# Optimization experiments

Measured on AMD Instinct MI355X. Metric: run time of the kernel, lower is better.

Reference implementation:

```python
import jax, jax.numpy as jnp
import numpy as np

B_COMMITMENT = 1.0


def setup_inputs() -> dict:
    key = jax.random.key(0)
    k1, k2 = jax.random.split(key)
    inpt = jax.random.normal(k1, (16, 1024, 256), dtype=jnp.float32)
    emb_mtrx = jax.random.normal(k2, (256, 8192), dtype=jnp.float32) * 0.05
    return {"inpt": inpt, "emb_mtrx": emb_mtrx}


def reference(inpt, emb_mtrx):
    D = inpt.shape[-1]
    x = inpt.reshape(-1, D)  # [N, D]
    # squared L2 distance to every code: [N, K]
    dist = (
        jnp.sum(x * x, axis=1, keepdims=True)
        - 2.0 * (x @ emb_mtrx)
        + jnp.sum(emb_mtrx * emb_mtrx, axis=0, keepdims=True)
    )
    idx = jnp.argmin(dist, axis=1).reshape(inpt.shape[:-1])  # [B, T]
    q = jnp.take(emb_mtrx.T, idx, axis=0)  # [B, T, D] gather of nearest codes
    l_commitment = jnp.mean((jax.lax.stop_gradient(q) - inpt) ** 2)
    l_codebook = jnp.mean((q - jax.lax.stop_gradient(inpt)) ** 2)
    loss = B_COMMITMENT * l_commitment + l_codebook
    q_st = inpt + jax.lax.stop_gradient(q - inpt)  # straight-through
    return q_st, loss
```

## Files before the change

### kernel.cpp

```cpp
#include <hip/hip_runtime.h>
#include <hip/hip_bf16.h>
#include <cstdint>


typedef __bf16 bf16x8 __attribute__((ext_vector_type(8)));
typedef __bf16 bf16x4 __attribute__((ext_vector_type(4)));
typedef float  f32x16 __attribute__((ext_vector_type(16)));

#define N_ROWS  16384
#define N_CODES 8192
#define DDIM    256
#define NT      16
#define BUFB    32768

#define STAGE16(gptr, lptr) __builtin_amdgcn_global_load_lds( \
    (const __attribute__((address_space(1))) void*)(gptr),    \
    (__attribute__((address_space(3))) void*)(lptr), 16, 0, 0)

#define SBAR() do { asm volatile("" ::: "memory"); \
                    __builtin_amdgcn_s_barrier();  \
                    asm volatile("" ::: "memory"); } while (0)
#define WAITVM(N) asm volatile("s_waitcnt vmcnt(" #N ")" ::: "memory")
#define LGKM0() do { asm volatile("s_waitcnt lgkmcnt(0)" ::: "memory"); \
                     __builtin_amdgcn_sched_barrier(0); } while (0)

__global__ void prep_x_k(const float* __restrict__ x,
                         __bf16* __restrict__ xhi, __bf16* __restrict__ xlo) {
  int i = blockIdx.x * 256 + threadIdx.x;
  float4 v = reinterpret_cast<const float4*>(x)[i];
  float a[4] = {v.x, v.y, v.z, v.w};
  bf16x4 h, l;
#pragma unroll
  for (int j = 0; j < 4; ++j) {
    __bf16 hh = (__bf16)a[j];
    h[j] = hh;
    l[j] = (__bf16)(a[j] - (float)hh);
  }
  reinterpret_cast<bf16x4*>(xhi)[i] = h;
  reinterpret_cast<bf16x4*>(xlo)[i] = l;
}

__global__ void prep_e_k(const float* __restrict__ emb,
                         __bf16* __restrict__ ehi, __bf16* __restrict__ elo,
                         float* __restrict__ embT) {
  __shared__ float tile[64][65];
  const int kb = blockIdx.x * 64, db = blockIdx.y * 64;
  const int t = threadIdx.x;
  const int tk = t & 63, td = t >> 6;
#pragma unroll
  for (int c = 0; c < 16; ++c) {
    int d = c * 4 + td;
    tile[d][tk] = emb[(size_t)(db + d) * N_CODES + kb + tk];
  }
  __syncthreads();
#pragma unroll
  for (int c = 0; c < 16; ++c) {
    int k = c * 4 + td;
    int d = tk;
    float v = tile[d][k];
    size_t o = (size_t)(kb + k) * DDIM + db + d;
    __bf16 h = (__bf16)v;
    embT[o] = v;
    ehi[o] = h;
    elo[o] = (__bf16)(v - (float)h);
  }
}

__global__ void enorm_k(const float* __restrict__ emb, float* __restrict__ enorm) {
  int k = blockIdx.x * 256 + threadIdx.x;
  float s = 0.f;
  for (int d = 0; d < DDIM; ++d) {
    float v = emb[(size_t)d * N_CODES + k];
    s += v * v;
  }
  enorm[k] = s;
}

__global__ __launch_bounds__(512, 2) void vq_main_k(
    const __bf16* __restrict__ xhi, const __bf16* __restrict__ xlo,
    const __bf16* __restrict__ ehi, const __bf16* __restrict__ elo,
    const float* __restrict__ enorm, unsigned long long* __restrict__ keys) {
  extern __shared__ __align__(16) unsigned char smem[];

  const int tid = threadIdx.x;
  const int wid = tid >> 6, lane = tid & 63;
  const int cg = wid >> 2, rg = wid & 3;
  const int l31 = lane & 31, lh = lane >> 5;

  const int orig = blockIdx.x;
  const int j = orig >> 3;
  const int bm = (orig & 7) * 8 + (j & 7);
  const int bn = j >> 3;

  const int cbase = bn * 256 + cg * 128 + lh * 4;
  f32x16 acc[4][2];
#pragma unroll
  for (int c = 0; c < 4; ++c) {
    f32x16 ci;
#pragma unroll
    for (int q = 0; q < 4; ++q)
#pragma unroll
      for (int r = 0; r < 4; ++r)
        ci[q * 4 + r] = -0.5f * enorm[cbase + c * 32 + q * 8 + r];
    acc[c][0] = ci; acc[c][1] = ci;
  }
  __builtin_amdgcn_sched_barrier(0);

  const size_t aoff = (size_t)(bm * 256 + wid * 32 + l31) * 512 + (size_t)lh * 16;
  const size_t boff = (size_t)(bn * 256 + wid * 32 + l31) * 512 + (size_t)lh * 16;
  const char* pxh = (const char*)xhi + aoff;
  const char* pxl = (const char*)xlo + aoff;
  const char* peh = (const char*)ehi + boff;
  const char* pel = (const char*)elo + boff;
  const int dxh = wid * 1024, dxl = 8192 + wid * 1024;
  const int deh = 16384 + wid * 1024, del = 24576 + wid * 1024;

  const int xrd = rg * 2048 + lane * 16;
  const int erd = 16384 + cg * 4096 + lane * 16;

  unsigned char* b0 = smem;
  unsigned char* b1 = smem + BUFB;
  unsigned char* b2 = smem + 2 * BUFB;

  STAGE16(pxh, b0 + dxh); STAGE16(peh, b0 + deh);
  STAGE16(pxl, b0 + dxl); STAGE16(pel, b0 + del);
  STAGE16(pxh + 32, b1 + dxh); STAGE16(peh + 32, b1 + deh);
  STAGE16(pxl + 32, b1 + dxl); STAGE16(pel + 32, b1 + del);
  WAITVM(4);
  SBAR();

#pragma unroll 1
  for (int t = 0; t < NT; ++t) {
    int s = t + 2; if (s >= NT) s -= NT;
    const size_t kb = (size_t)s * 32;

    bf16x8 ehf[4], xhf[2];
#pragma unroll
    for (int c = 0; c < 4; ++c) ehf[c] = *(const bf16x8*)(b0 + erd + c * 1024);
#pragma unroll
    for (int r = 0; r < 2; ++r) xhf[r] = *(const bf16x8*)(b0 + xrd + r * 1024);
    STAGE16(pxh + kb, b2 + dxh);
    STAGE16(peh + kb, b2 + deh);
    SBAR();
    LGKM0();
    __builtin_amdgcn_s_setprio(1);
#pragma unroll
    for (int c = 0; c < 4; ++c)
#pragma unroll
      for (int r = 0; r < 2; ++r)
        acc[c][r] = __builtin_amdgcn_mfma_f32_32x32x16_bf16(ehf[c], xhf[r], acc[c][r], 0, 0, 0);
    __builtin_amdgcn_s_setprio(0);
    SBAR();

    bf16x8 xlf[2];
#pragma unroll
    for (int r = 0; r < 2; ++r) xlf[r] = *(const bf16x8*)(b0 + 8192 + xrd + r * 1024);
    STAGE16(pxl + kb, b2 + dxl);
    SBAR();
    LGKM0();
    __builtin_amdgcn_s_setprio(1);
#pragma unroll
    for (int c = 0; c < 4; ++c)
#pragma unroll
      for (int r = 0; r < 2; ++r)
        acc[c][r] = __builtin_amdgcn_mfma_f32_32x32x16_bf16(ehf[c], xlf[r], acc[c][r], 0, 0, 0);
    __builtin_amdgcn_s_setprio(0);
    SBAR();

    bf16x8 elf[4];
#pragma unroll
    for (int c = 0; c < 4; ++c) elf[c] = *(const bf16x8*)(b0 + 8192 + erd + c * 1024);
    STAGE16(pel + kb, b2 + del);
    SBAR();
    LGKM0();
    __builtin_amdgcn_s_setprio(1);
#pragma unroll
    for (int c = 0; c < 4; ++c)
#pragma unroll
      for (int r = 0; r < 2; ++r)
        acc[c][r] = __builtin_amdgcn_mfma_f32_32x32x16_bf16(elf[c], xhf[r], acc[c][r], 0, 0, 0);
    __builtin_amdgcn_s_setprio(0);
    WAITVM(4);
    SBAR();

    unsigned char* bt = b0; b0 = b1; b1 = b2; b2 = bt;
  }
  WAITVM(0);

#pragma unroll
  for (int r = 0; r < 2; ++r) {
    float bv = -3.4e38f;
    unsigned bcode = 0;
#pragma unroll
    for (int c = 0; c < 4; ++c)
#pragma unroll
      for (int q = 0; q < 4; ++q)
#pragma unroll
        for (int rr = 0; rr < 4; ++rr) {
          float v = acc[c][r][q * 4 + rr];
          unsigned cd = (unsigned)(cbase + c * 32 + q * 8 + rr);
          if (v > bv) { bv = v; bcode = cd; }
        }
    unsigned u = __float_as_uint(bv);
    u = (u & 0x80000000u) ? ~u : (u | 0x80000000u);
    unsigned long long key =
        ((unsigned long long)u << 32) | (unsigned)(0xFFFFFFFFu ^ bcode);
    unsigned olo = __shfl_xor((unsigned)key, 32, 64);
    unsigned ohi = __shfl_xor((unsigned)(key >> 32), 32, 64);
    unsigned long long okey = ((unsigned long long)ohi << 32) | olo;
    if (okey > key) key = okey;
    if (lane < 32)
      atomicMax(&keys[bm * 256 + rg * 64 + r * 32 + l31], key);
  }
}

__global__ void gather_k(const float* __restrict__ x, const float* __restrict__ embT,
                         const unsigned long long* __restrict__ keys,
                         float* __restrict__ qout, float* __restrict__ rowsum) {
  const int row = blockIdx.x;
  const int lane = threadIdx.x;
  const unsigned low = (unsigned)(keys[row] & 0xffffffffull);
  const int idx = (int)(~low);
  float4 q  = reinterpret_cast<const float4*>(embT + (size_t)idx * DDIM)[lane];
  float4 xv = reinterpret_cast<const float4*>(x + (size_t)row * DDIM)[lane];
  reinterpret_cast<float4*>(qout + (size_t)row * DDIM)[lane] = q;
  float dx = q.x - xv.x, dy = q.y - xv.y, dz = q.z - xv.z, dw = q.w - xv.w;
  float s = dx * dx + dy * dy + dz * dz + dw * dw;
#pragma unroll
  for (int mk = 32; mk; mk >>= 1) s += __shfl_xor(s, mk, 64);
  if (lane == 0) rowsum[row] = s;
}

__global__ void loss_k(const float* __restrict__ rowsum, float* __restrict__ out) {
  __shared__ float sm[4];
  const int t = threadIdx.x;
  float s = 0.f;
  for (int j = t; j < N_ROWS; j += 256) s += rowsum[j];
#pragma unroll
  for (int mk = 32; mk; mk >>= 1) s += __shfl_xor(s, mk, 64);
  if ((t & 63) == 0) sm[t >> 6] = s;
  __syncthreads();
  if (t == 0) out[0] = 2.0f * (sm[0] + sm[1] + sm[2] + sm[3]) / (float)(N_ROWS * DDIM);
}

extern "C" void kernel_launch(void* const* d_in, const int* in_sizes, int n_in,
                              void* d_out, int out_size, void* d_ws, size_t ws_size,
                              hipStream_t stream) {
  const float* x   = (const float*)d_in[0];
  const float* emb = (const float*)d_in[1];
  float* qout = (float*)d_out;

  char* w = (char*)d_ws;
  unsigned long long* keys = (unsigned long long*)w;
  float* rowsum = (float*)(w + 131072);
  __bf16* xhi = (__bf16*)(w + 196608);
  __bf16* xlo = xhi + (size_t)N_ROWS * DDIM;
  __bf16* ehi = xlo + (size_t)N_ROWS * DDIM;
  __bf16* elo = ehi + (size_t)N_CODES * DDIM;
  float*  embT = (float*)(elo + (size_t)N_CODES * DDIM);
  float*  enorm = embT + (size_t)N_CODES * DDIM;

  hipFuncSetAttribute((const void*)vq_main_k,
                      hipFuncAttributeMaxDynamicSharedMemorySize, 3 * BUFB);

  hipMemsetAsync(keys, 0, N_ROWS * sizeof(unsigned long long), stream);
  prep_x_k<<<4096, 256, 0, stream>>>(x, xhi, xlo);
  prep_e_k<<<dim3(N_CODES / 64, DDIM / 64), 256, 0, stream>>>(emb, ehi, elo, embT);
  enorm_k<<<N_CODES / 256, 256, 0, stream>>>(emb, enorm);
  vq_main_k<<<2048, 512, 3 * BUFB, stream>>>(xhi, xlo, ehi, elo, enorm, keys);
  gather_k<<<N_ROWS, 64, 0, stream>>>(x, embT, keys, qout, rowsum);
  loss_k<<<1, 256, 0, stream>>>(rowsum, qout + (size_t)N_ROWS * DDIM);
}
```

Baseline: 246.2 us.

## Add bf16-only first pass with margin-based rescue of ambiguous rows

Replaces the single split-precision (hi+lo) distance GEMM with a hi-only bf16 pass that tracks the top two scores per row. Rows whose winning margin exceeds a fixed threshold are accepted directly. The remaining rows, up to a cap, are compacted and recomputed with the full hi/lo precision kernel. The fp32 transposed codebook copy is dropped and gather rebuilds codes from hi+lo. This cuts roughly two thirds of the MFMA work for confident rows, at the cost of extra kernels and a heuristic threshold that could mis-assign rows when bf16 error exceeds the margin.

Measured after the change: 239.4 us. 2.8% less time.

```diff
diff --git a/kernel.cpp b/kernel.cpp
--- a/kernel.cpp
+++ b/kernel.cpp
@@ -11,7 +11,10 @@
 #define N_CODES 8192
 #define DDIM    256
 #define NT      16
-#define BUFB    32768
+#define BUFB1   16384
+#define BUFB3   32768
+#define NMAX    8192
+#define THETA   0.025f
 
 #define STAGE16(gptr, lptr) __builtin_amdgcn_global_load_lds( \
     (const __attribute__((address_space(1))) void*)(gptr),    \
@@ -24,6 +27,15 @@
 #define LGKM0() do { asm volatile("s_waitcnt lgkmcnt(0)" ::: "memory"); \
                      __builtin_amdgcn_sched_barrier(0); } while (0)
 
+__device__ __forceinline__ unsigned mapf(float f) {
+  unsigned u = __float_as_uint(f);
+  return (u & 0x80000000u) ? ~u : (u | 0x80000000u);
+}
+__device__ __forceinline__ float unmapf(unsigned u) {
+  u = (u & 0x80000000u) ? (u & 0x7fffffffu) : ~u;
+  return __uint_as_float(u);
+}
+
 __global__ void prep_x_k(const float* __restrict__ x,
                          __bf16* __restrict__ xhi, __bf16* __restrict__ xlo) {
   int i = blockIdx.x * 256 + threadIdx.x;
@@ -41,8 +53,7 @@
 }
 
 __global__ void prep_e_k(const float* __restrict__ emb,
-                         __bf16* __restrict__ ehi, __bf16* __restrict__ elo,
-                         float* __restrict__ embT) {
+                         __bf16* __restrict__ ehi, __bf16* __restrict__ elo) {
   __shared__ float tile[64][65];
   const int kb = blockIdx.x * 64, db = blockIdx.y * 64;
   const int t = threadIdx.x;
@@ -60,7 +71,6 @@
     float v = tile[d][k];
     size_t o = (size_t)(kb + k) * DDIM + db + d;
     __bf16 h = (__bf16)v;
-    embT[o] = v;
     ehi[o] = h;
     elo[o] = (__bf16)(v - (float)h);
   }
@@ -76,11 +86,11 @@
   enorm[k] = s;
 }
 
-__global__ __launch_bounds__(512, 2) void vq_main_k(
-    const __bf16* __restrict__ xhi, const __bf16* __restrict__ xlo,
-    const __bf16* __restrict__ ehi, const __bf16* __restrict__ elo,
-    const float* __restrict__ enorm, unsigned long long* __restrict__ keys) {
-  extern __shared__ __align__(16) unsigned char smem[];
+__global__ __launch_bounds__(512, 2) void pass1_k(
+    const __bf16* __restrict__ xhi, const __bf16* __restrict__ ehi,
+    const float* __restrict__ enorm,
+    unsigned long long* __restrict__ k2k, float* __restrict__ k2v) {
+  __shared__ alignas(16) unsigned char smem[3][BUFB1];
 
   const int tid = threadIdx.x;
   const int wid = tid >> 6, lane = tid & 63;
@@ -109,7 +119,167 @@
   const size_t aoff = (size_t)(bm * 256 + wid * 32 + l31) * 512 + (size_t)lh * 16;
   const size_t boff = (size_t)(bn * 256 + wid * 32 + l31) * 512 + (size_t)lh * 16;
   const char* pxh = (const char*)xhi + aoff;
-  const char* pxl = (const char*)xlo + aoff;
+  const char* peh = (const char*)ehi + boff;
+  const int dxh = wid * 1024, deh = 8192 + wid * 1024;
+
+  const int xrd = rg * 2048 + lane * 16;
+  const int erd = 8192 + cg * 4096 + lane * 16;
+
+  unsigned char* b0 = &smem[0][0];
+  unsigned char* b1 = &smem[1][0];
+  unsigned char* b2 = &smem[2][0];
+
+  STAGE16(pxh, b0 + dxh); STAGE16(peh, b0 + deh);
+  STAGE16(pxh + 32, b1 + dxh); STAGE16(peh + 32, b1 + deh);
+  WAITVM(2);
+  SBAR();
+
+#pragma unroll 1
+  for (int t = 0; t < NT; ++t) {
+    int s = t + 2; if (s >= NT) s -= NT;
+    const size_t kb = (size_t)s * 32;
+
+    bf16x8 ehf[4], xhf[2];
+#pragma unroll
+    for (int c = 0; c < 4; ++c) ehf[c] = *(const bf16x8*)(b0 + erd + c * 1024);
+#pragma unroll
+    for (int r = 0; r < 2; ++r) xhf[r] = *(const bf16x8*)(b0 + xrd + r * 1024);
+    STAGE16(pxh + kb, b2 + dxh);
+    STAGE16(peh + kb, b2 + deh);
+    SBAR();
+    LGKM0();
+    __builtin_amdgcn_s_setprio(1);
+#pragma unroll
+    for (int c = 0; c < 4; ++c)
+#pragma unroll
+      for (int r = 0; r < 2; ++r)
+        acc[c][r] = __builtin_amdgcn_mfma_f32_32x32x16_bf16(ehf[c], xhf[r], acc[c][r], 0, 0, 0);
+    __builtin_amdgcn_s_setprio(0);
+    WAITVM(2);
+    SBAR();
+    unsigned char* bt = b0; b0 = b1; b1 = b2; b2 = bt;
+  }
+  WAITVM(0);
+  SBAR();
+
+  unsigned long long* ek = (unsigned long long*)&smem[0][0];
+  float* ev = (float*)(&smem[0][0] + 2048);
+  const int rowl = rg * 64 + l31;
+
+#pragma unroll
+  for (int r = 0; r < 2; ++r) {
+    float v1 = -3.4e38f, v2 = -3.4e38f;
+    unsigned c1 = 0;
+#pragma unroll
+    for (int c = 0; c < 4; ++c)
+#pragma unroll
+      for (int q = 0; q < 4; ++q)
+#pragma unroll
+        for (int rr = 0; rr < 4; ++rr) {
+          float v = acc[c][r][q * 4 + rr];
+          unsigned cd = (unsigned)(cbase + c * 32 + q * 8 + rr);
+          if (v > v1) { v2 = v1; v1 = v; c1 = cd; }
+          else if (v > v2) v2 = v;
+        }
+    unsigned long long key =
+        ((unsigned long long)mapf(v1) << 32) | (0xFFFFFFFFu ^ c1);
+    unsigned klo = (unsigned)key, khi = (unsigned)(key >> 32);
+    unsigned plo = __shfl_xor(klo, 32, 64), phi = __shfl_xor(khi, 32, 64);
+    float pv1 = __shfl_xor(v1, 32, 64), pv2 = __shfl_xor(v2, 32, 64);
+    unsigned long long pkey = ((unsigned long long)phi << 32) | plo;
+    if (pkey > key) { v2 = fmaxf(v1, pv2); v1 = pv1; key = pkey; }
+    else { v2 = fmaxf(pv1, v2); }
+    SBAR();
+    if (cg == 1 && lh == 0) { ek[rowl + r * 32] = key; ev[rowl + r * 32] = v2; }
+    SBAR();
+    if (cg == 0 && lh == 0) {
+      unsigned long long pk = ek[rowl + r * 32];
+      float ps2 = ev[rowl + r * 32];
+      float nv2;
+      if (pk > key) { nv2 = fmaxf(v1, ps2); key = pk; }
+      else nv2 = fmaxf(unmapf((unsigned)(pk >> 32)), v2);
+      const int grow = bm * 256 + rowl + r * 32;
+      k2k[(size_t)bn * N_ROWS + grow] = key;
+      k2v[(size_t)bn * N_ROWS + grow] = nv2;
+    }
+  }
+}
+
+__global__ void reduce_k(const unsigned long long* __restrict__ k2k,
+                         const float* __restrict__ k2v,
+                         unsigned long long* __restrict__ keys,
+                         unsigned* __restrict__ counter,
+                         int* __restrict__ idxlist) {
+  const int row = blockIdx.x * 256 + threadIdx.x;
+  unsigned long long k = k2k[row];
+  float s2 = k2v[row];
+#pragma unroll 1
+  for (int p = 1; p < 32; ++p) {
+    unsigned long long kk = k2k[(size_t)p * N_ROWS + row];
+    float ss2 = k2v[(size_t)p * N_ROWS + row];
+    if (kk > k) { s2 = fmaxf(unmapf((unsigned)(k >> 32)), ss2); k = kk; }
+    else        { s2 = fmaxf(unmapf((unsigned)(kk >> 32)), s2); }
+  }
+  float v1 = unmapf((unsigned)(k >> 32));
+  if (v1 - s2 >= THETA) {
+    keys[row] = k;
+  } else {
+    keys[row] = 0;
+    unsigned pos = atomicAdd(counter, 1u);
+    if (pos < NMAX) idxlist[pos] = row;
+    else keys[row] = k;
+  }
+}
+
+__global__ void compact_k(const __bf16* __restrict__ xhi, const __bf16* __restrict__ xlo,
+                          const int* __restrict__ idxlist, const unsigned* __restrict__ counter,
+                          __bf16* __restrict__ xch, __bf16* __restrict__ xcl) {
+  const unsigned b = blockIdx.x;
+  if (b >= *counter) return;
+  const int row = idxlist[b];
+  const int lane = threadIdx.x;
+  reinterpret_cast<uint2*>(xch)[(size_t)b * 64 + lane] =
+      reinterpret_cast<const uint2*>(xhi)[(size_t)row * 64 + lane];
+  reinterpret_cast<uint2*>(xcl)[(size_t)b * 64 + lane] =
+      reinterpret_cast<const uint2*>(xlo)[(size_t)row * 64 + lane];
+}
+
+__global__ __launch_bounds__(512, 2) void rescue_k(
+    const __bf16* __restrict__ xch, const __bf16* __restrict__ xcl,
+    const __bf16* __restrict__ ehi, const __bf16* __restrict__ elo,
+    const float* __restrict__ enorm, unsigned long long* __restrict__ keys,
+    const int* __restrict__ idxlist, const unsigned* __restrict__ counter) {
+  extern __shared__ __align__(16) unsigned char smem[];
+
+  const int bm = blockIdx.x >> 5;
+  const int bn = blockIdx.x & 31;
+  const unsigned nf = *counter;
+  const int tiles = (int)((nf + 255u) >> 8);
+  if (bm >= tiles) return;
+
+  const int tid = threadIdx.x;
+  const int wid = tid >> 6, lane = tid & 63;
+  const int cg = wid >> 2, rg = wid & 3;
+  const int l31 = lane & 31, lh = lane >> 5;
+
+  const int cbase = bn * 256 + cg * 128 + lh * 4;
+  f32x16 acc[4][2];
+#pragma unroll
+  for (int c = 0; c < 4; ++c) {
+    f32x16 ci;
+#pragma unroll
+    for (int q = 0; q < 4; ++q)
+#pragma unroll
+      for (int r = 0; r < 4; ++r)
+        ci[q * 4 + r] = -0.5f * enorm[cbase + c * 32 + q * 8 + r];
+    acc[c][0] = ci; acc[c][1] = ci;
+  }
+  __builtin_amdgcn_sched_barrier(0);
+
+  const size_t aoff = (size_t)(bm * 256 + wid * 32 + l31) * 512 + (size_t)lh * 16;
+  const size_t boff = (size_t)(bn * 256 + wid * 32 + l31) * 512 + (size_t)lh * 16;
+  const char* pxh = (const char*)xch + aoff;
+  const char* pxl = (const char*)xcl + aoff;
   const char* peh = (const char*)ehi + boff;
   const char* pel = (const char*)elo + boff;
   const int dxh = wid * 1024, dxl = 8192 + wid * 1024;
@@ -119,8 +289,8 @@
   const int erd = 16384 + cg * 4096 + lane * 16;
 
   unsigned char* b0 = smem;
-  unsigned char* b1 = smem + BUFB;
-  unsigned char* b2 = smem + 2 * BUFB;
+  unsigned char* b1 = smem + BUFB3;
+  unsigned char* b2 = smem + 2 * BUFB3;
 
   STAGE16(pxh, b0 + dxh); STAGE16(peh, b0 + deh);
   STAGE16(pxl, b0 + dxl); STAGE16(pel, b0 + del);
@@ -201,28 +371,34 @@
           unsigned cd = (unsigned)(cbase + c * 32 + q * 8 + rr);
           if (v > bv) { bv = v; bcode = cd; }
         }
-    unsigned u = __float_as_uint(bv);
-    u = (u & 0x80000000u) ? ~u : (u | 0x80000000u);
     unsigned long long key =
-        ((unsigned long long)u << 32) | (unsigned)(0xFFFFFFFFu ^ bcode);
+        ((unsigned long long)mapf(bv) << 32) | (0xFFFFFFFFu ^ bcode);
     unsigned olo = __shfl_xor((unsigned)key, 32, 64);
     unsigned ohi = __shfl_xor((unsigned)(key >> 32), 32, 64);
     unsigned long long okey = ((unsigned long long)ohi << 32) | olo;
     if (okey > key) key = okey;
-    if (lane < 32)
-      atomicMax(&keys[bm * 256 + rg * 64 + r * 32 + l31], key);
-  }
-}
-
-__global__ void gather_k(const float* __restrict__ x, const float* __restrict__ embT,
+    const int crow = bm * 256 + rg * 64 + r * 32 + l31;
+    if (lane < 32 && crow < (int)nf)
+      atomicMax(&keys[idxlist[crow]], key);
+  }
+}
+
+__global__ void gather_k(const float* __restrict__ x,
+                         const __bf16* __restrict__ ehi, const __bf16* __restrict__ elo,
                          const unsigned long long* __restrict__ keys,
                          float* __restrict__ qout, float* __restrict__ rowsum) {
   const int row = blockIdx.x;
   const int lane = threadIdx.x;
   const unsigned low = (unsigned)(keys[row] & 0xffffffffull);
   const int idx = (int)(~low);
-  float4 q  = reinterpret_cast<const float4*>(embT + (size_t)idx * DDIM)[lane];
+  ushort4 h4 = reinterpret_cast<const ushort4*>(ehi + (size_t)idx * DDIM)[lane];
+  ushort4 l4 = reinterpret_cast<const ushort4*>(elo + (size_t)idx * DDIM)[lane];
   float4 xv = reinterpret_cast<const float4*>(x + (size_t)row * DDIM)[lane];
+  float4 q;
+  q.x = __uint_as_float((unsigned)h4.x << 16) + __uint_as_float((unsigned)l4.x << 16);
+  q.y = __uint_as_float((unsigned)h4.y << 16) + __uint_as_float((unsigned)l4.y << 16);
+  q.z = __uint_as_float((unsigned)h4.z << 16) + __uint_as_float((unsigned)l4.z << 16);
+  q.w = __uint_as_float((unsigned)h4.w << 16) + __uint_as_float((unsigned)l4.w << 16);
   reinterpret_cast<float4*>(qout + (size_t)row * DDIM)[lane] = q;
   float dx = q.x - xv.x, dy = q.y - xv.y, dz = q.z - xv.z, dw = q.w - xv.w;
   float s = dx * dx + dy * dy + dz * dz + dw * dw;
@@ -252,22 +428,32 @@
 
   char* w = (char*)d_ws;
   unsigned long long* keys = (unsigned long long*)w;
-  float* rowsum = (float*)(w + 131072);
-  __bf16* xhi = (__bf16*)(w + 196608);
-  __bf16* xlo = xhi + (size_t)N_ROWS * DDIM;
-  __bf16* ehi = xlo + (size_t)N_ROWS * DDIM;
-  __bf16* elo = ehi + (size_t)N_CODES * DDIM;
-  float*  embT = (float*)(elo + (size_t)N_CODES * DDIM);
-  float*  enorm = embT + (size_t)N_CODES * DDIM;
-
-  hipFuncSetAttribute((const void*)vq_main_k,
-                      hipFuncAttributeMaxDynamicSharedMemorySize, 3 * BUFB);
-
-  hipMemsetAsync(keys, 0, N_ROWS * sizeof(unsigned long long), stream);
+  float* rowsum   = (float*)(w + 131072);
+  unsigned* counter = (unsigned*)(w + 196608);
+  int* idxlist    = (int*)(w + 197632);
+  __bf16* xhi     = (__bf16*)(w + 262144);
+  __bf16* xlo     = xhi + (size_t)N_ROWS * DDIM;
+  __bf16* ehi     = xlo + (size_t)N_ROWS * DDIM;
+  __bf16* elo     = ehi + (size_t)N_CODES * DDIM;
+  float*  enorm   = (float*)(elo + (size_t)N_CODES * DDIM);
+  char*   k2base  = (char*)(enorm + N_CODES);
+  unsigned long long* k2k = (unsigned long long*)k2base;
+  float*  k2v     = (float*)(k2base + 4194304);
+  __bf16* xch     = (__bf16*)k2base;
+  __bf16* xcl     = (__bf16*)(k2base + 4194304);
+
+  hipFuncSetAttribute((const void*)rescue_k,
+                      hipFuncAttributeMaxDynamicSharedMemorySize, 3 * BUFB3);
+
+  hipMemsetAsync(counter, 0, sizeof(unsigned), stream);
   prep_x_k<<<4096, 256, 0, stream>>>(x, xhi, xlo);
-  prep_e_k<<<dim3(N_CODES / 64, DDIM / 64), 256, 0, stream>>>(emb, ehi, elo, embT);
+  prep_e_k<<<dim3(N_CODES / 64, DDIM / 64), 256, 0, stream>>>(emb, ehi, elo);
   enorm_k<<<N_CODES / 256, 256, 0, stream>>>(emb, enorm);
-  vq_main_k<<<2048, 512, 3 * BUFB, stream>>>(xhi, xlo, ehi, elo, enorm, keys);
-  gather_k<<<N_ROWS, 64, 0, stream>>>(x, embT, keys, qout, rowsum);
+  pass1_k<<<2048, 512, 0, stream>>>(xhi, ehi, enorm, k2k, k2v);
+  reduce_k<<<N_ROWS / 256, 256, 0, stream>>>(k2k, k2v, keys, counter, idxlist);
+  compact_k<<<NMAX, 64, 0, stream>>>(xhi, xlo, idxlist, counter, xch, xcl);
+  rescue_k<<<(NMAX / 256) * 32, 512, 3 * BUFB3, stream>>>(
+      xch, xcl, ehi, elo, enorm, keys, idxlist, counter);
+  gather_k<<<N_ROWS, 64, 0, stream>>>(x, ehi, elo, keys, qout, rowsum);
   loss_k<<<1, 256, 0, stream>>>(rowsum, qout + (size_t)N_ROWS * DDIM);
 }
```
